# Kernel optimization log

Measured on AMD Instinct MI355X. Metric: run time of the kernel, lower is better.

The kernel has to match this reference:

```python
import jax, jax.numpy as jnp
import numpy as np

TEMPERATURE = 0.5
EPS = 1e-8  # torch F.cosine_similarity eps


def _neg_mask_indices(two_b):
    """Static row/col indices replicating sim[mask].view(2B, -1).
    Mask excludes the diagonal and the (i, B+i)/(B+i, i) positive pairs,
    leaving exactly 2B-2 entries per row, extracted in row-major order."""
    b = two_b // 2
    mask = np.ones((two_b, two_b), dtype=bool)
    np.fill_diagonal(mask, False)
    i = np.arange(b)
    mask[i, b + i] = False
    mask[b + i, i] = False
    rows, cols = np.nonzero(mask)
    return rows.reshape(two_b, two_b - 2), cols.reshape(two_b, two_b - 2)


def setup_inputs() -> dict:
    key = jax.random.key(0)
    k1, k2 = jax.random.split(key)
    two_b, d = 8192, 128
    embeddings = jax.random.normal(k1, (two_b, d), dtype=jnp.float32)
    labels = jax.random.randint(k2, (two_b,), 0, two_b - 2)
    return {"embeddings": embeddings, "labels": labels}


def reference(embeddings, labels):
    two_b = embeddings.shape[0]
    # cosine similarity via normalize + matmul (same math as the broadcast
    # F.cosine_similarity, without the O(N^2*D) intermediate)
    norms = jnp.linalg.norm(embeddings, axis=1)  # [2B]
    sim = (embeddings @ embeddings.T) / jnp.maximum(norms[:, None] * norms[None, :], EPS)
    sim = sim / TEMPERATURE  # [2B, 2B]
    rows, cols = _neg_mask_indices(two_b)
    logits = sim[rows, cols]  # [2B, 2B-2]
    # CrossEntropyLoss(reduction='sum') then / (2B)
    logz = jax.nn.logsumexp(logits, axis=1)  # [2B]
    picked = jnp.take_along_axis(logits, labels[:, None].astype(jnp.int32), axis=1)[:, 0]
    loss = jnp.sum(logz - picked) / two_b
    return loss
```

## Files before the change

kernel.cpp:

```cpp
#include <hip/hip_runtime.h>
#include <hip/hip_bf16.h>


typedef __bf16 bf16x8 __attribute__((ext_vector_type(8)));
typedef float floatx4 __attribute__((ext_vector_type(4)));

#define TWO_B 8192
#define B_HALF 4096
#define D 128
#define INV_T 2.0f
#define FIXED_MAX 2.0f
#define C_EXP 2.885390081777927f

#if defined(__has_builtin) && __has_builtin(__builtin_amdgcn_exp2f)
#define EXP2F(x) __builtin_amdgcn_exp2f(x)
#else
#define EXP2F(x) exp2f(x)
#endif
#if defined(__has_builtin) && __has_builtin(__builtin_amdgcn_logf)
#define LOG2F(x) __builtin_amdgcn_logf(x)
#else
#define LOG2F(x) log2f(x)
#endif

__device__ inline void load16_lds(const __bf16* g, __bf16* l) {
    __builtin_amdgcn_global_load_lds(
        (const __attribute__((address_space(1))) unsigned int*)g,
        (__attribute__((address_space(3))) unsigned int*)l, 16, 0, 0);
}

__global__ void k_prep(const float* __restrict__ emb,
                       const int* __restrict__ labels,
                       __bf16* __restrict__ nb,
                       float* __restrict__ picked,
                       float* __restrict__ l_arr) {
    int wv   = threadIdx.x >> 6;
    int lane = threadIdx.x & 63;
    int i = blockIdx.x * 4 + wv;
    const float2* e2 = reinterpret_cast<const float2*>(emb + (size_t)i * D);
    float2 v = e2[lane];
    float ssi = v.x * v.x + v.y * v.y;
    int p = i ^ B_HALF;
    int a = min(i, p), b = max(i, p);
    int l = labels[i];
    int c = l + (l >= a);
    c += (c >= b);
    const float2* ec2 = reinterpret_cast<const float2*>(emb + (size_t)c * D);
    float2 u = ec2[lane];
    float dot = v.x * u.x + v.y * u.y;
    float ssc = u.x * u.x + u.y * u.y;
#pragma unroll
    for (int off = 32; off >= 1; off >>= 1) {
        ssi += __shfl_xor(ssi, off, 64);
        dot += __shfl_xor(dot, off, 64);
        ssc += __shfl_xor(ssc, off, 64);
    }
    float rn = rsqrtf(fmaxf(ssi, 1e-16f));
    union { __bf16 h[2]; unsigned int uu; } pk;
    pk.h[0] = (__bf16)(v.x * rn);
    pk.h[1] = (__bf16)(v.y * rn);
    reinterpret_cast<unsigned int*>(nb)[i * 64 + lane] = pk.uu;
    if (lane == 0)
        picked[i] = dot / fmaxf(sqrtf(ssi * ssc), 1e-8f) * INV_T;
    if (blockIdx.x < TWO_B / 256) l_arr[blockIdx.x * 256 + threadIdx.x] = 0.f;
}

__global__ __launch_bounds__(256, 4) void k_gemm(const __bf16* __restrict__ nb,
                                                 float* __restrict__ l_arr) {
    __shared__ __bf16 lds[16384];

    const int bi = blockIdx.x;
    const int g  = blockIdx.y;

    const int lane = threadIdx.x & 63;
    const int w    = threadIdx.x >> 6;
    const int m    = lane & 15;
    const int quad = lane >> 4;
    const int row0 = bi * 128 + w * 32;

    bf16x8 a0[4], a1[4];
#pragma unroll
    for (int kc = 0; kc < 4; ++kc) {
        a0[kc] = *reinterpret_cast<const bf16x8*>(
            nb + (size_t)(row0 + m) * D + kc * 32 + quad * 8);
        a1[kc] = *reinterpret_cast<const bf16x8*>(
            nb + (size_t)(row0 + 16 + m) * D + kc * 32 + quad * 8);
    }
    asm volatile("" : "+v"(a0[0]), "+v"(a0[1]), "+v"(a0[2]), "+v"(a0[3]),
                      "+v"(a1[0]), "+v"(a1[1]), "+v"(a1[2]), "+v"(a1[3]));

    float l0[4] = {0.f, 0.f, 0.f, 0.f};
    float l1[4] = {0.f, 0.f, 0.f, 0.f};
    const int i0 = row0 + quad * 4;

    bool first = true;
#pragma unroll
    for (int si = 0; si < 2; ++si) {
        const int by = g + si * 17;
        if (by > 32) continue;
        if (by == 32 && bi >= 32) continue;
        const int bj = (bi + by) & 63;
        const int C0 = bj * 128;
        const bool isdiag = (by == 0);
        const bool bmask = isdiag || (by == 32);

        if (!first) __syncthreads();
        first = false;

        {
            const __bf16* gp = nb + (size_t)(C0 + m) * D + w * 32 + quad * 8;
#pragma unroll
            for (int j = 0; j < 8; ++j)
                load16_lds(gp + (size_t)j * 16 * D, &lds[j * 2048 + w * 512]);
        }
        __syncthreads();

        float csum[8];
#pragma unroll
        for (int grp = 0; grp < 2; ++grp) {
            floatx4 acc0[4] = {{0.f,0.f,0.f,0.f},{0.f,0.f,0.f,0.f},
                               {0.f,0.f,0.f,0.f},{0.f,0.f,0.f,0.f}};
            floatx4 acc1[4] = {{0.f,0.f,0.f,0.f},{0.f,0.f,0.f,0.f},
                               {0.f,0.f,0.f,0.f},{0.f,0.f,0.f,0.f}};
#pragma unroll
            for (int kc = 0; kc < 4; ++kc) {
                const bf16x8 a0k = a0[kc], a1k = a1[kc];
#pragma unroll
                for (int s = 0; s < 4; ++s) {
                    bf16x8 b = *reinterpret_cast<const bf16x8*>(
                        &lds[((grp * 4 + s) * 4 + kc) * 512 + lane * 8]);
                    acc0[s] = __builtin_amdgcn_mfma_f32_16x16x32_bf16(a0k, b, acc0[s], 0, 0, 0);
                    acc1[s] = __builtin_amdgcn_mfma_f32_16x16x32_bf16(a1k, b, acc1[s], 0, 0, 0);
                }
            }
#pragma unroll
            for (int s = 0; s < 4; ++s) {
                const int jj = C0 + (grp * 4 + s) * 16 + m;
                float cs = 0.f;
                if (bmask) {
#pragma unroll
                    for (int r = 0; r < 4; ++r) {
                        float e0 = EXP2F(fmaf(acc0[s][r], C_EXP, -C_EXP));
                        float e1 = EXP2F(fmaf(acc1[s][r], C_EXP, -C_EXP));
                        if (((jj ^ (i0 + r)) & ~B_HALF) == 0) e0 = 0.f;
                        if (((jj ^ (i0 + 16 + r)) & ~B_HALF) == 0) e1 = 0.f;
                        l0[r] += e0;
                        l1[r] += e1;
                        cs += e0 + e1;
                    }
                } else {
#pragma unroll
                    for (int r = 0; r < 4; ++r) {
                        float e0 = EXP2F(fmaf(acc0[s][r], C_EXP, -C_EXP));
                        float e1 = EXP2F(fmaf(acc1[s][r], C_EXP, -C_EXP));
                        l0[r] += e0;
                        l1[r] += e1;
                        cs += e0 + e1;
                    }
                }
                cs += __shfl_xor(cs, 16, 64);
                cs += __shfl_xor(cs, 32, 64);
                csum[grp * 4 + s] = cs;
            }
        }

        if (!isdiag) {
            __syncthreads();
            float* ldsf = reinterpret_cast<float*>(lds);
            if (quad == 0) {
#pragma unroll
                for (int sub = 0; sub < 8; ++sub)
                    ldsf[w * 128 + sub * 16 + m] = csum[sub];
            }
            __syncthreads();
            if (threadIdx.x < 128) {
                float t = ldsf[threadIdx.x] + ldsf[128 + threadIdx.x] +
                          ldsf[256 + threadIdx.x] + ldsf[384 + threadIdx.x];
                atomicAdd(&l_arr[C0 + threadIdx.x], t);
            }
        }
    }

#pragma unroll
    for (int r = 0; r < 4; ++r) {
        float s = l0[r];
        s += __shfl_xor(s, 1, 64);
        s += __shfl_xor(s, 2, 64);
        s += __shfl_xor(s, 4, 64);
        s += __shfl_xor(s, 8, 64);
        if (m == 0) atomicAdd(&l_arr[i0 + r], s);
    }
#pragma unroll
    for (int r = 0; r < 4; ++r) {
        float s = l1[r];
        s += __shfl_xor(s, 1, 64);
        s += __shfl_xor(s, 2, 64);
        s += __shfl_xor(s, 4, 64);
        s += __shfl_xor(s, 8, 64);
        if (m == 0) atomicAdd(&l_arr[i0 + 16 + r], s);
    }
}

__global__ void k_final(const float* __restrict__ l_arr,
                        const float* __restrict__ picked,
                        float* __restrict__ out) {
    __shared__ float sred[16];
    float s = 0.f;
#pragma unroll
    for (int k = 0; k < TWO_B / 1024; ++k) {
        int i = threadIdx.x + k * 1024;
        s += FIXED_MAX + LOG2F(l_arr[i]) * 0.6931471805599453f - picked[i];
    }
#pragma unroll
    for (int off = 32; off >= 1; off >>= 1) s += __shfl_xor(s, off, 64);
    if ((threadIdx.x & 63) == 0) sred[threadIdx.x >> 6] = s;
    __syncthreads();
    if (threadIdx.x == 0) {
        float t = 0.f;
#pragma unroll
        for (int k = 0; k < 16; ++k) t += sred[k];
        out[0] = t * (1.0f / TWO_B);
    }
}

extern "C" void kernel_launch(void* const* d_in, const int* in_sizes, int n_in,
                              void* d_out, int out_size, void* d_ws, size_t ws_size,
                              hipStream_t stream) {
    const float* emb    = (const float*)d_in[0];
    const int*   labels = (const int*)d_in[1];
    char* ws = (char*)d_ws;
    float*  l_arr  = (float*)ws;
    float*  picked = (float*)(ws + 32768);
    __bf16* nb     = (__bf16*)(ws + 65536);
    float*  out    = (float*)d_out;

    k_prep<<<TWO_B / 4, 256, 0, stream>>>(emb, labels, nb, picked, l_arr);
    dim3 g2(64, 17);
    k_gemm<<<g2, 256, 0, stream>>>(nb, l_arr);
    k_final<<<1, 1024, 0, stream>>>(l_arr, picked, out);
}
```

Baseline: 83.92 us.

## Load B tiles directly from global into registers, drop LDS staging and barriers

Removes the LDS staging of the column tile and all __syncthreads; each wave now loads its B fragments straight from global memory (L2/L1-cached) per 16-column sub-tile. The column sums are atomically added per wave instead of being reduced through LDS first. This is meant to cut barrier and LDS traffic, but it quadruples global/L1 reads of B (each of four waves reads the full tile) and increases atomic traffic fourfold.

```diff
diff --git a/kernel.cpp b/kernel.cpp
--- a/kernel.cpp
+++ b/kernel.cpp
@@ -22,12 +22,6 @@
 #else
 #define LOG2F(x) log2f(x)
 #endif
-
-__device__ inline void load16_lds(const __bf16* g, __bf16* l) {
-    __builtin_amdgcn_global_load_lds(
-        (const __attribute__((address_space(1))) unsigned int*)g,
-        (__attribute__((address_space(3))) unsigned int*)l, 16, 0, 0);
-}
 
 __global__ void k_prep(const float* __restrict__ emb,
                        const int* __restrict__ labels,
@@ -67,8 +61,6 @@
 
 __global__ __launch_bounds__(256, 4) void k_gemm(const __bf16* __restrict__ nb,
                                                  float* __restrict__ l_arr) {
-    __shared__ __bf16 lds[16384];
-
     const int bi = blockIdx.x;
     const int g  = blockIdx.y;
 
@@ -93,7 +85,6 @@
     float l1[4] = {0.f, 0.f, 0.f, 0.f};
     const int i0 = row0 + quad * 4;
 
-    bool first = true;
 #pragma unroll
     for (int si = 0; si < 2; ++si) {
         const int by = g + si * 17;
@@ -104,79 +95,54 @@
         const bool isdiag = (by == 0);
         const bool bmask = isdiag || (by == 32);
 
-        if (!first) __syncthreads();
-        first = false;
-
-        {
-            const __bf16* gp = nb + (size_t)(C0 + m) * D + w * 32 + quad * 8;
-#pragma unroll
-            for (int j = 0; j < 8; ++j)
-                load16_lds(gp + (size_t)j * 16 * D, &lds[j * 2048 + w * 512]);
-        }
-        __syncthreads();
-
-        float csum[8];
-#pragma unroll
-        for (int grp = 0; grp < 2; ++grp) {
-            floatx4 acc0[4] = {{0.f,0.f,0.f,0.f},{0.f,0.f,0.f,0.f},
-                               {0.f,0.f,0.f,0.f},{0.f,0.f,0.f,0.f}};
-            floatx4 acc1[4] = {{0.f,0.f,0.f,0.f},{0.f,0.f,0.f,0.f},
-                               {0.f,0.f,0.f,0.f},{0.f,0.f,0.f,0.f}};
-#pragma unroll
-            for (int kc = 0; kc < 4; ++kc) {
-                const bf16x8 a0k = a0[kc], a1k = a1[kc];
-#pragma unroll
-                for (int s = 0; s < 4; ++s) {
-                    bf16x8 b = *reinterpret_cast<const bf16x8*>(
-                        &lds[((grp * 4 + s) * 4 + kc) * 512 + lane * 8]);
-                    acc0[s] = __builtin_amdgcn_mfma_f32_16x16x32_bf16(a0k, b, acc0[s], 0, 0, 0);
-                    acc1[s] = __builtin_amdgcn_mfma_f32_16x16x32_bf16(a1k, b, acc1[s], 0, 0, 0);
+        const __bf16* bp = nb + (size_t)(C0 + m) * D + quad * 8;
+
+#pragma unroll
+        for (int sub = 0; sub < 8; ++sub) {
+            const __bf16* bs = bp + (size_t)sub * 16 * D;
+            bf16x8 b0 = *reinterpret_cast<const bf16x8*>(bs);
+            bf16x8 b1 = *reinterpret_cast<const bf16x8*>(bs + 32);
+            bf16x8 b2 = *reinterpret_cast<const bf16x8*>(bs + 64);
+            bf16x8 b3 = *reinterpret_cast<const bf16x8*>(bs + 96);
+
+            floatx4 acc0 = {0.f, 0.f, 0.f, 0.f};
+            floatx4 acc1 = {0.f, 0.f, 0.f, 0.f};
+            acc0 = __builtin_amdgcn_mfma_f32_16x16x32_bf16(a0[0], b0, acc0, 0, 0, 0);
+            acc1 = __builtin_amdgcn_mfma_f32_16x16x32_bf16(a1[0], b0, acc1, 0, 0, 0);
+            acc0 = __builtin_amdgcn_mfma_f32_16x16x32_bf16(a0[1], b1, acc0, 0, 0, 0);
+            acc1 = __builtin_amdgcn_mfma_f32_16x16x32_bf16(a1[1], b1, acc1, 0, 0, 0);
+            acc0 = __builtin_amdgcn_mfma_f32_16x16x32_bf16(a0[2], b2, acc0, 0, 0, 0);
+            acc1 = __builtin_amdgcn_mfma_f32_16x16x32_bf16(a1[2], b2, acc1, 0, 0, 0);
+            acc0 = __builtin_amdgcn_mfma_f32_16x16x32_bf16(a0[3], b3, acc0, 0, 0, 0);
+            acc1 = __builtin_amdgcn_mfma_f32_16x16x32_bf16(a1[3], b3, acc1, 0, 0, 0);
+
+            const int jj = C0 + sub * 16 + m;
+            float cs = 0.f;
+            if (bmask) {
+#pragma unroll
+                for (int r = 0; r < 4; ++r) {
+                    float e0 = EXP2F(fmaf(acc0[r], C_EXP, -C_EXP));
+                    float e1 = EXP2F(fmaf(acc1[r], C_EXP, -C_EXP));
+                    if (((jj ^ (i0 + r)) & ~B_HALF) == 0) e0 = 0.f;
+                    if (((jj ^ (i0 + 16 + r)) & ~B_HALF) == 0) e1 = 0.f;
+                    l0[r] += e0;
+                    l1[r] += e1;
+                    cs += e0 + e1;
+                }
+            } else {
+#pragma unroll
+                for (int r = 0; r < 4; ++r) {
+                    float e0 = EXP2F(fmaf(acc0[r], C_EXP, -C_EXP));
+                    float e1 = EXP2F(fmaf(acc1[r], C_EXP, -C_EXP));
+                    l0[r] += e0;
+                    l1[r] += e1;
+                    cs += e0 + e1;
                 }
             }
-#pragma unroll
-            for (int s = 0; s < 4; ++s) {
-                const int jj = C0 + (grp * 4 + s) * 16 + m;
-                float cs = 0.f;
-                if (bmask) {
-#pragma unroll
-                    for (int r = 0; r < 4; ++r) {
-                        float e0 = EXP2F(fmaf(acc0[s][r], C_EXP, -C_EXP));
-                        float e1 = EXP2F(fmaf(acc1[s][r], C_EXP, -C_EXP));
-                        if (((jj ^ (i0 + r)) & ~B_HALF) == 0) e0 = 0.f;
-                        if (((jj ^ (i0 + 16 + r)) & ~B_HALF) == 0) e1 = 0.f;
-                        l0[r] += e0;
-                        l1[r] += e1;
-                        cs += e0 + e1;
-                    }
-                } else {
-#pragma unroll
-                    for (int r = 0; r < 4; ++r) {
-                        float e0 = EXP2F(fmaf(acc0[s][r], C_EXP, -C_EXP));
-                        float e1 = EXP2F(fmaf(acc1[s][r], C_EXP, -C_EXP));
-                        l0[r] += e0;
-                        l1[r] += e1;
-                        cs += e0 + e1;
-                    }
-                }
+            if (!isdiag) {
                 cs += __shfl_xor(cs, 16, 64);
                 cs += __shfl_xor(cs, 32, 64);
-                csum[grp * 4 + s] = cs;
-            }
-        }
-
-        if (!isdiag) {
-            __syncthreads();
-            float* ldsf = reinterpret_cast<float*>(lds);
-            if (quad == 0) {
-#pragma unroll
-                for (int sub = 0; sub < 8; ++sub)
-                    ldsf[w * 128 + sub * 16 + m] = csum[sub];
-            }
-            __syncthreads();
-            if (threadIdx.x < 128) {
-                float t = ldsf[threadIdx.x] + ldsf[128 + threadIdx.x] +
-                          ldsf[256 + threadIdx.x] + ldsf[384 + threadIdx.x];
-                atomicAdd(&l_arr[C0 + threadIdx.x], t);
+                if (quad == 0) atomicAdd(&l_arr[jj], cs);
             }
         }
     }
```

Result: slower. 105.0 us (+25.1%).

## Double-buffer column strips in LDS and replace block reduction with per-wave atomics

Applied to the files above, without the earlier changes.

Issues the global-to-LDS loads for both column strips up front into two LDS buffers, then waits with partial vmcnt counts so compute on the first strip overlaps the second strip's load. It also drops the LDS-based cross-wave column-sum reduction and its extra barriers, and has each wave atomically add its column sums directly. LDS per block doubles and the launch-bounds occupancy hint drops from 4 to 2 blocks. Global atomics per block rise roughly fourfold.

```diff
diff --git a/kernel.cpp b/kernel.cpp
--- a/kernel.cpp
+++ b/kernel.cpp
@@ -65,9 +65,9 @@
     if (blockIdx.x < TWO_B / 256) l_arr[blockIdx.x * 256 + threadIdx.x] = 0.f;
 }
 
-__global__ __launch_bounds__(256, 4) void k_gemm(const __bf16* __restrict__ nb,
+__global__ __launch_bounds__(256, 2) void k_gemm(const __bf16* __restrict__ nb,
                                                  float* __restrict__ l_arr) {
-    __shared__ __bf16 lds[16384];
+    __shared__ __bf16 lds[2][16384];
 
     const int bi = blockIdx.x;
     const int g  = blockIdx.y;
@@ -93,29 +93,27 @@
     float l1[4] = {0.f, 0.f, 0.f, 0.f};
     const int i0 = row0 + quad * 4;
 
-    bool first = true;
-#pragma unroll
-    for (int si = 0; si < 2; ++si) {
-        const int by = g + si * 17;
-        if (by > 32) continue;
-        if (by == 32 && bi >= 32) continue;
-        const int bj = (bi + by) & 63;
-        const int C0 = bj * 128;
-        const bool isdiag = (by == 0);
-        const bool bmask = isdiag || (by == 32);
-
-        if (!first) __syncthreads();
-        first = false;
-
-        {
-            const __bf16* gp = nb + (size_t)(C0 + m) * D + w * 32 + quad * 8;
+    const int by0 = g;
+    const int bj0 = (bi + by0) & 63;
+    const bool has1 = (g + 17 <= 32) && !((g + 17 == 32) && (bi >= 32));
+    const int by1 = g + 17;
+    const int bj1 = (bi + by1) & 63;
+
+    {
+        const __bf16* gp0 = nb + (size_t)(bj0 * 128 + m) * D + w * 32 + quad * 8;
+#pragma unroll
+        for (int j = 0; j < 8; ++j)
+            load16_lds(gp0 + (size_t)j * 16 * D, &lds[0][j * 2048 + w * 512]);
+        if (has1) {
+            const __bf16* gp1 = nb + (size_t)(bj1 * 128 + m) * D + w * 32 + quad * 8;
 #pragma unroll
             for (int j = 0; j < 8; ++j)
-                load16_lds(gp + (size_t)j * 16 * D, &lds[j * 2048 + w * 512]);
+                load16_lds(gp1 + (size_t)j * 16 * D, &lds[1][j * 2048 + w * 512]);
         }
-        __syncthreads();
-
-        float csum[8];
+    }
+    __builtin_amdgcn_sched_barrier(0);
+
+    auto compute_strip = [&](int C0, bool isdiag, bool bmask, const __bf16* buf) {
 #pragma unroll
         for (int grp = 0; grp < 2; ++grp) {
             floatx4 acc0[4] = {{0.f,0.f,0.f,0.f},{0.f,0.f,0.f,0.f},
@@ -128,7 +126,7 @@
 #pragma unroll
                 for (int s = 0; s < 4; ++s) {
                     bf16x8 b = *reinterpret_cast<const bf16x8*>(
-                        &lds[((grp * 4 + s) * 4 + kc) * 512 + lane * 8]);
+                        &buf[((grp * 4 + s) * 4 + kc) * 512 + lane * 8]);
                     acc0[s] = __builtin_amdgcn_mfma_f32_16x16x32_bf16(a0k, b, acc0[s], 0, 0, 0);
                     acc1[s] = __builtin_amdgcn_mfma_f32_16x16x32_bf16(a1k, b, acc1[s], 0, 0, 0);
                 }
@@ -158,27 +156,26 @@
                         cs += e0 + e1;
                     }
                 }
-                cs += __shfl_xor(cs, 16, 64);
-                cs += __shfl_xor(cs, 32, 64);
-                csum[grp * 4 + s] = cs;
+                if (!isdiag) {
+                    cs += __shfl_xor(cs, 16, 64);
+                    cs += __shfl_xor(cs, 32, 64);
+                    if (quad == 0) atomicAdd(&l_arr[jj], cs);
+                }
             }
         }
-
-        if (!isdiag) {
-            __syncthreads();
-            float* ldsf = reinterpret_cast<float*>(lds);
-            if (quad == 0) {
-#pragma unroll
-                for (int sub = 0; sub < 8; ++sub)
-                    ldsf[w * 128 + sub * 16 + m] = csum[sub];
-            }
-            __syncthreads();
-            if (threadIdx.x < 128) {
-                float t = ldsf[threadIdx.x] + ldsf[128 + threadIdx.x] +
-                          ldsf[256 + threadIdx.x] + ldsf[384 + threadIdx.x];
-                atomicAdd(&l_arr[C0 + threadIdx.x], t);
-            }
-        }
+    };
+
+    if (has1) { asm volatile("s_waitcnt vmcnt(8)" ::: "memory"); }
+    else      { asm volatile("s_waitcnt vmcnt(0)" ::: "memory"); }
+    __builtin_amdgcn_s_barrier();
+    __builtin_amdgcn_sched_barrier(0);
+    compute_strip(bj0 * 128, by0 == 0, (by0 == 0) || (by0 == 32), &lds[0][0]);
+
+    if (has1) {
+        asm volatile("s_waitcnt vmcnt(0)" ::: "memory");
+        __builtin_amdgcn_s_barrier();
+        __builtin_amdgcn_sched_barrier(0);
+        compute_strip(bj1 * 128, false, (by1 == 32), &lds[1][0]);
     }
 
 #pragma unroll
```

Result: slower. 88.53 us (+5.5%).
